# Optimization experiments

Hardware: AMD Instinct MI355X
Metric: run time of the kernel (lower is better)

The kernel has to match this reference:

```python
import jax, jax.numpy as jnp
import numpy as np

NEG = -1e20

def _rope(x):
    # x: (N, L, H, D). Original buffers use inv_freq over D with D/2 entries;
    # sin/cos tiled to full D to broadcast (original code's einsum was under-specified for 4D).
    L, D = x.shape[1], x.shape[3]
    inv_freq = 1.0 / (10000.0 ** (jnp.arange(0, D, 2, dtype=jnp.float32) / D))
    t = jnp.arange(L, dtype=jnp.float32)
    freqs = t[:, None] * inv_freq[None, :]            # (L, D/2)
    sin = jnp.concatenate([jnp.sin(freqs)] * 2, -1)[None, :, None, :]  # (1,L,1,D)
    cos = jnp.concatenate([jnp.cos(freqs)] * 2, -1)[None, :, None, :]
    return x * cos + jnp.flip(x, -1) * sin

def setup_inputs() -> dict:
    key = jax.random.key(0)
    ks = jax.random.split(key, 8)
    N, L, E, H = 2, 1024, 2048, 16
    D = E // H
    s = 0.02
    return {
        "values": jax.random.normal(ks[0], (N, L, E), jnp.float32),
        "keys": jax.random.normal(ks[1], (N, L, E), jnp.float32),
        "queries": jax.random.normal(ks[2], (N, L, E), jnp.float32),
        "mask": jax.random.randint(ks[3], (N, 1, L, L), 0, 2, jnp.int32),
        "Wv": jax.random.normal(ks[4], (D, D), jnp.float32) * s,
        "Wk": jax.random.normal(ks[5], (D, D), jnp.float32) * s,
        "Wq": jax.random.normal(ks[6], (D, D), jnp.float32) * s,
        "Wo": jax.random.normal(ks[7], (E, E), jnp.float32) * s,
        "bo": jnp.zeros((E,), jnp.float32),
    }

def reference(values, keys, queries, mask, Wv, Wk, Wq, Wo, bo):
    N, L, E = queries.shape
    H = 16
    D = E // H
    v = values.reshape(N, L, H, D)
    k = keys.reshape(N, L, H, D)
    q = queries.reshape(N, L, H, D)
    q = _rope(q)
    k = _rope(k)
    # per-head linears (nn.Linear: x @ W.T)
    v = jnp.einsum('nlhd,od->nlho', v, Wv)
    k = jnp.einsum('nlhd,od->nlho', k, Wk)
    q = jnp.einsum('nlhd,od->nlho', q, Wq)
    energy = jnp.einsum('nqhd,nkhd->nhqk', q, k)
    energy = jnp.where(mask == 0, NEG, energy)
    attn = jax.nn.softmax(energy / jnp.sqrt(jnp.float32(E)), axis=3)
    out = jnp.einsum('nhqk,nkhd->nqhd', attn, v).reshape(N, L, E)
    return out @ Wo.T + bo
```

## Files before the change

### kernel.cpp

```cpp
#include <hip/hip_runtime.h>

#define LQ 1024
#define EMB 2048
#define NH 16
#define HD 128
#define RSCALE 0.022097086912079608f

typedef unsigned short u16x8 __attribute__((ext_vector_type(8)));
typedef __bf16 bf16x8 __attribute__((ext_vector_type(8)));
typedef float f32x4 __attribute__((ext_vector_type(4)));
typedef short s16x4 __attribute__((ext_vector_type(4)));

typedef const __attribute__((address_space(1))) unsigned int* gas_t;
typedef __attribute__((address_space(3))) unsigned int* las_t;

__device__ __forceinline__ void glds16(const void* g, void* l){
  __builtin_amdgcn_global_load_lds((gas_t)g, (las_t)l, 16, 0, 0);
}
__device__ __forceinline__ unsigned short f2b(float f){
  unsigned int x = __float_as_uint(f);
  return (unsigned short)((x + 0x7fffu + ((x >> 16) & 1u)) >> 16);
}
__device__ __forceinline__ short f2bs(float f){
  union { __bf16 h; short s; } c; c.h = (__bf16)f; return c.s;
}
__device__ __forceinline__ bf16x8 as_bf(u16x8 u){
  union { u16x8 u; bf16x8 b; } c; c.u = u; return c.b;
}
__device__ __forceinline__ f32x4 mfma16(s16x4 a, s16x4 b, f32x4 c){
  return __builtin_amdgcn_mfma_f32_16x16x16bf16_1k(a, b, c, 0, 0, 0);
}

__global__ __launch_bounds__(256) void k_prep(const float* __restrict__ Wo,
                                              unsigned short* __restrict__ Wob,
                                              const int* __restrict__ M,
                                              unsigned long long* __restrict__ Mb){
  int bx = blockIdx.x, t = threadIdx.x;
  if (bx < 4096) {
    int i = (bx * 256 + t) * 4;
    float4 f = *(const float4*)&Wo[i];
    ushort4 u;
    u.x = f2b(f.x); u.y = f2b(f.y); u.z = f2b(f.z); u.w = f2b(f.w);
    *(ushort4*)&Wob[i] = u;
  } else {
    int w_idx = (bx - 4096) * 4 + (t >> 6);
    int lane = t & 63;
    int n = w_idx >> 14, row = (w_idx >> 4) & 1023, wc = w_idx & 15;
    int v = M[(size_t)n * (LQ * LQ) + (size_t)row * LQ + wc * 64 + lane];
    unsigned long long b = __ballot(v != 0);
    if (lane == 0) Mb[w_idx] = b;
  }
}

__global__ __launch_bounds__(256) void k_proj(
    const float* __restrict__ vals, const float* __restrict__ keys,
    const float* __restrict__ qrys,
    const float* __restrict__ Wv, const float* __restrict__ Wk,
    const float* __restrict__ Wq,
    unsigned short* __restrict__ vp, unsigned short* __restrict__ kp,
    unsigned short* __restrict__ qp)
{
  __shared__ unsigned short Xs[64 * 136];
  __shared__ unsigned short Ws[128 * 136];
  __shared__ float scC[4 * 128], scS[4 * 128];
  int t = threadIdx.x;
  int which = blockIdx.y;
  const float* X; const float* W; unsigned short* OUT; bool rope;
  if (which == 0)      { X = vals; W = Wv; OUT = vp; rope = false; }
  else if (which == 1) { X = keys; W = Wk; OUT = kp; rope = true;  }
  else                 { X = qrys; W = Wq; OUT = qp; rope = true;  }
  float qs = (which == 2) ? RSCALE : 1.0f;
  int m0 = blockIdx.x * 64;

  #pragma unroll
  for (int i = 0; i < 8; ++i) {
    int ci = t + 256 * i;
    int row = ci >> 4, ch = ci & 15;
    float4 a = *(const float4*)&W[row * 128 + ch * 8];
    float4 b = *(const float4*)&W[row * 128 + ch * 8 + 4];
    u16x8 u;
    u[0]=f2b(a.x); u[1]=f2b(a.y); u[2]=f2b(a.z); u[3]=f2b(a.w);
    u[4]=f2b(b.x); u[5]=f2b(b.y); u[6]=f2b(b.z); u[7]=f2b(b.w);
    *(u16x8*)&Ws[row * 136 + ch * 8] = u;
  }
  if (rope) {
    int l0 = (blockIdx.x * 4) & 1023;
    #pragma unroll
    for (int i = 0; i < 2; ++i) {
      int idx = t + 256 * i;
      int li = idx >> 7, d = idx & 127, j = d & 63;
      float inv = 1.0f / powf(10000.0f, (float)(2 * j) * 0.0078125f);
      float ang = (float)(l0 + li) * inv;
      scC[idx] = cosf(ang);
      scS[idx] = sinf(ang);
    }
  }
  __syncthreads();
  #pragma unroll
  for (int i = 0; i < 8; ++i) {
    int fi = t + 256 * i;
    int row = fi >> 5, dq = (fi & 31) * 4;
    int gr = m0 + row;
    float4 x = *(const float4*)&X[(size_t)gr * HD + dq];
    ushort4 u;
    if (rope) {
      int li = row >> 4;
      float4 xm = *(const float4*)&X[(size_t)gr * HD + (124 - dq)];
      float4 c  = *(const float4*)&scC[li * 128 + dq];
      float4 s  = *(const float4*)&scS[li * 128 + dq];
      u.x = f2b(x.x * c.x + xm.w * s.x);
      u.y = f2b(x.y * c.y + xm.z * s.y);
      u.z = f2b(x.z * c.z + xm.y * s.z);
      u.w = f2b(x.w * c.w + xm.x * s.w);
    } else {
      u.x = f2b(x.x); u.y = f2b(x.y); u.z = f2b(x.z); u.w = f2b(x.w);
    }
    *(ushort4*)&Xs[row * 136 + dq] = u;
  }
  __syncthreads();

  int w = t >> 6, lane = t & 63, quad = lane >> 4, n16 = lane & 15;
  f32x4 of[4][2];
  #pragma unroll
  for (int a = 0; a < 4; ++a)
    { of[a][0] = (f32x4){0.f,0.f,0.f,0.f}; of[a][1] = (f32x4){0.f,0.f,0.f,0.f}; }

  #pragma unroll
  for (int kd = 0; kd < 4; ++kd) {
    bf16x8 bfr[2];
    #pragma unroll
    for (int b2 = 0; b2 < 2; ++b2)
      bfr[b2] = as_bf(*(const u16x8*)&Ws[(w * 32 + b2 * 16 + n16) * 136 + kd * 32 + quad * 8]);
    #pragma unroll
    for (int a = 0; a < 4; ++a) {
      bf16x8 af = as_bf(*(const u16x8*)&Xs[(a * 16 + n16) * 136 + kd * 32 + quad * 8]);
      of[a][0] = __builtin_amdgcn_mfma_f32_16x16x32_bf16(af, bfr[0], of[a][0], 0, 0, 0);
      of[a][1] = __builtin_amdgcn_mfma_f32_16x16x32_bf16(af, bfr[1], of[a][1], 0, 0, 0);
    }
  }

  #pragma unroll
  for (int a = 0; a < 4; ++a) {
    #pragma unroll
    for (int b2 = 0; b2 < 2; ++b2) {
      #pragma unroll
      for (int r = 0; r < 4; ++r) {
        int m = m0 + a * 16 + quad * 4 + r;
        int n = m >> 14, l = (m >> 4) & 1023, h = m & 15;
        int o = w * 32 + b2 * 16 + n16;
        OUT[(((size_t)(n * NH + h)) * LQ + l) * HD + o] = f2b(of[a][b2][r] * qs);
      }
    }
  }
}

__global__ __launch_bounds__(256) void k_vtrans(const unsigned short* __restrict__ vp,
                                                unsigned short* __restrict__ vtF){
  __shared__ unsigned short Ls[64 * 136];
  int t = threadIdx.x;
  int kt = blockIdx.x;
  int l0 = kt * 64;
  size_t base = (size_t)blockIdx.y * LQ * HD;
  #pragma unroll
  for (int i = 0; i < 4; ++i) {
    int ci = t + 256 * i;
    int row = ci >> 4, ch = ci & 15;
    *(u16x8*)&Ls[row * 136 + ch * 8] =
        *(const u16x8*)&vp[base + (size_t)(l0 + row) * HD + ch * 8];
  }
  __syncthreads();
  #pragma unroll
  for (int i = 0; i < 4; ++i) {
    int m = t + 256 * i;
    int b = m >> 5, w5 = m & 31;
    int c = b >> 3, c2 = b & 7;
    int l1 = 2 * w5;
    int qd = l1 >> 4, nn0 = l1 & 15;
    u16x8 pk;
    #pragma unroll
    for (int j = 0; j < 4; ++j)
      pk[j] = Ls[(c * 16 + qd * 4 + j) * 136 + c2 * 16 + nn0];
    #pragma unroll
    for (int j = 0; j < 4; ++j)
      pk[4 + j] = Ls[(c * 16 + qd * 4 + j) * 136 + c2 * 16 + nn0 + 1];
    *(u16x8*)&vtF[base + (size_t)kt * 8192 + (size_t)m * 8] = pk;
  }
}

__global__ __launch_bounds__(512) void k_attn(
    const unsigned short* __restrict__ qp, const unsigned short* __restrict__ kp,
    const unsigned short* __restrict__ vtF, const unsigned long long* __restrict__ Mb,
    unsigned short* __restrict__ ao)
{
  __shared__ unsigned short KsF[2][8192];
  __shared__ unsigned short VsF[2][8192];
  __shared__ float ls[8][16];
  int t = threadIdx.x, w = t >> 6, lane = t & 63, quad = lane >> 4, n16 = lane & 15;
  int grp = w >> 2, wq = w & 3;
  int lin = blockIdx.y * gridDim.x + blockIdx.x;
  int xcd = lin & 7, j = lin >> 3;
  int bh = xcd + 8 * (j >> 4);
  int q0 = (j & 15) * 64;
  int nIdx = bh >> 4, h = bh & 15;
  size_t base = (size_t)bh * LQ * HD;
  const unsigned short* Q = qp + base;
  const unsigned short* K = kp + base;
  const unsigned short* VF = vtF + base;

  bf16x8 qf[4];
  #pragma unroll
  for (int kd = 0; kd < 4; ++kd)
    qf[kd] = as_bf(*(const u16x8*)&Q[(size_t)(q0 + wq * 16 + n16) * HD + kd * 32 + quad * 8]);

  const unsigned long long* MbRow =
      Mb + ((size_t)nIdx * LQ + q0 + wq * 16 + n16) * 16;

  f32x4 of[8];
  #pragma unroll
  for (int c = 0; c < 8; ++c) of[c] = (f32x4){0.f, 0.f, 0.f, 0.f};
  float lp = 0.f;

  for (int p = 0; p < 8; ++p) {
    int k0 = p * 128;
    __syncthreads();
    #pragma unroll
    for (int jj = 0; jj < 2; ++jj) {
      int kt = 2 * p + jj;
      #pragma unroll
      for (int i = 0; i < 2; ++i) {
        int D = t + 512 * i;
        int nn = D & 15, qq = (D >> 4) & 3, cc = (D >> 6) & 3, kd = D >> 8;
        glds16(&K[(size_t)(k0 + jj * 64 + cc * 16 + nn) * HD + (kd * 4 + qq) * 8],
               &KsF[jj][(size_t)D * 8]);
        glds16(&VF[(size_t)kt * 8192 + (size_t)D * 8],
               &VsF[jj][(size_t)D * 8]);
      }
    }
    unsigned long long mq = MbRow[2 * p + grp];
    __syncthreads();

    unsigned long long msh = mq >> (quad * 4);

    f32x4 sf[4];
    #pragma unroll
    for (int c = 0; c < 4; ++c) sf[c] = (f32x4){0.f, 0.f, 0.f, 0.f};
    __builtin_amdgcn_s_setprio(1);
    #pragma unroll
    for (int kd = 0; kd < 4; ++kd) {
      #pragma unroll
      for (int c = 0; c < 4; ++c) {
        bf16x8 kv = as_bf(*(const u16x8*)&KsF[grp][((kd * 4 + c) * 64 + lane) * 8]);
        sf[c] = __builtin_amdgcn_mfma_f32_16x16x32_bf16(kv, qf[kd], sf[c], 0, 0, 0);
      }
    }
    __builtin_amdgcn_s_setprio(0);
    #pragma unroll
    for (int c = 0; c < 4; ++c) {
      s16x4 pa;
      #pragma unroll
      for (int r = 0; r < 4; ++r) {
        int bit = (int)((msh >> (c * 16 + r)) & 1ull);
        float p = bit ? __expf(sf[c][r]) : 0.f;
        lp += p;
        pa[r] = f2bs(p);
      }
      __builtin_amdgcn_s_setprio(1);
      #pragma unroll
      for (int c2 = 0; c2 < 8; ++c2) {
        s16x4 vv = *(const s16x4*)&VsF[grp][((c * 8 + c2) * 64 + lane) * 4];
        of[c2] = mfma16(pa, vv, of[c2]);
      }
      __builtin_amdgcn_s_setprio(0);
    }
  }

  __syncthreads();
  {
    float s = lp;
    s += __shfl_xor(s, 16);
    s += __shfl_xor(s, 32);
    ls[w][n16] = s;
  }
  float* OF = (float*)&KsF[0][0];
  if (grp == 1) {
    #pragma unroll
    for (int c2 = 0; c2 < 8; ++c2) {
      #pragma unroll
      for (int r = 0; r < 4; ++r) {
        OF[(wq * 16 + quad * 4 + r) * 128 + c2 * 16 + n16] = of[c2][r];
      }
    }
  }
  __syncthreads();
  if (grp == 0) {
    float linv[4];
    #pragma unroll
    for (int r = 0; r < 4; ++r)
      linv[r] = 1.0f / fmaxf(ls[wq][quad * 4 + r] + ls[wq + 4][quad * 4 + r], 1e-30f);
    #pragma unroll
    for (int c2 = 0; c2 < 8; ++c2) {
      #pragma unroll
      for (int r = 0; r < 4; ++r) {
        float v = of[c2][r] + OF[(wq * 16 + quad * 4 + r) * 128 + c2 * 16 + n16];
        ao[((size_t)(nIdx * LQ + q0 + wq * 16 + quad * 4 + r)) * EMB + h * HD + c2 * 16 + n16] =
            f2b(v * linv[r]);
      }
    }
  }
}

__global__ __launch_bounds__(256) void k_outproj(
    const unsigned short* __restrict__ ao, const unsigned short* __restrict__ Wob,
    const float* __restrict__ bo, float* __restrict__ out)
{
  __shared__ unsigned short As[2][128 * 64];
  __shared__ unsigned short Bs[2][64 * 64];
  int t = threadIdx.x;
  int w = t >> 6, lane = t & 63, quad = lane >> 4, n16 = lane & 15;
  int wm = w >> 1, wo = w & 1;
  int m0 = blockIdx.x * 128, o0 = blockIdx.y * 64;
  int ub = (t & 192);

  f32x4 of[4][2];
  #pragma unroll
  for (int a = 0; a < 4; ++a)
    { of[a][0] = (f32x4){0.f,0.f,0.f,0.f}; of[a][1] = (f32x4){0.f,0.f,0.f,0.f}; }

  #pragma unroll
  for (int i = 0; i < 4; ++i) {
    int ci = t + 256 * i;
    int row = ci >> 3, ch = (ci & 7) ^ (row & 7);
    glds16(&ao[(size_t)(m0 + row) * EMB + ch * 8], &As[0][(ub + 256 * i) * 8]);
  }
  #pragma unroll
  for (int i = 0; i < 2; ++i) {
    int ci = t + 256 * i;
    int row = ci >> 3, ch = (ci & 7) ^ (row & 7);
    glds16(&Wob[(size_t)(o0 + row) * EMB + ch * 8], &Bs[0][(ub + 256 * i) * 8]);
  }

  for (int kt = 0; kt < 32; ++kt) {
    int cur = kt & 1;
    __syncthreads();
    if (kt < 31) {
      int k1 = (kt + 1) * 64;
      #pragma unroll
      for (int i = 0; i < 4; ++i) {
        int ci = t + 256 * i;
        int row = ci >> 3, ch = (ci & 7) ^ (row & 7);
        glds16(&ao[(size_t)(m0 + row) * EMB + k1 + ch * 8], &As[1 - cur][(ub + 256 * i) * 8]);
      }
      #pragma unroll
      for (int i = 0; i < 2; ++i) {
        int ci = t + 256 * i;
        int row = ci >> 3, ch = (ci & 7) ^ (row & 7);
        glds16(&Wob[(size_t)(o0 + row) * EMB + k1 + ch * 8], &Bs[1 - cur][(ub + 256 * i) * 8]);
      }
    }
    #pragma unroll
    for (int kd = 0; kd < 2; ++kd) {
      int slot0 = (kd * 4 + quad);
      bf16x8 af[4], bf[2];
      #pragma unroll
      for (int a = 0; a < 4; ++a)
        af[a] = as_bf(*(const u16x8*)&As[cur][(wm * 64 + a * 16 + n16) * 64 + (slot0 ^ (n16 & 7)) * 8]);
      #pragma unroll
      for (int b = 0; b < 2; ++b)
        bf[b] = as_bf(*(const u16x8*)&Bs[cur][(wo * 32 + b * 16 + n16) * 64 + (slot0 ^ (n16 & 7)) * 8]);
      #pragma unroll
      for (int a = 0; a < 4; ++a)
        #pragma unroll
        for (int b = 0; b < 2; ++b)
          of[a][b] = __builtin_amdgcn_mfma_f32_16x16x32_bf16(af[a], bf[b], of[a][b], 0, 0, 0);
    }
  }

  float bb[2] = { bo[o0 + wo * 32 + n16], bo[o0 + wo * 32 + 16 + n16] };
  #pragma unroll
  for (int a = 0; a < 4; ++a) {
    #pragma unroll
    for (int b = 0; b < 2; ++b) {
      #pragma unroll
      for (int r = 0; r < 4; ++r) {
        out[(size_t)(m0 + wm * 64 + a * 16 + quad * 4 + r) * EMB
            + o0 + wo * 32 + b * 16 + n16] = of[a][b][r] + bb[b];
      }
    }
  }
}

extern "C" void kernel_launch(void* const* d_in, const int* in_sizes, int n_in,
                              void* d_out, int out_size, void* d_ws, size_t ws_size,
                              hipStream_t stream) {
  (void)in_sizes; (void)n_in; (void)out_size; (void)ws_size;
  const float* vals = (const float*)d_in[0];
  const float* keys = (const float*)d_in[1];
  const float* qrys = (const float*)d_in[2];
  const int*   mask = (const int*)d_in[3];
  const float* Wv   = (const float*)d_in[4];
  const float* Wk   = (const float*)d_in[5];
  const float* Wq   = (const float*)d_in[6];
  const float* Wo   = (const float*)d_in[7];
  const float* bo   = (const float*)d_in[8];
  float* out = (float*)d_out;

  unsigned short* U  = (unsigned short*)d_ws;
  unsigned short* qp = U;
  unsigned short* kp = U + 4194304;
  unsigned short* vp = U + 8388608;
  unsigned short* vtF= U + 12582912;
  unsigned short* ao = U + 16777216;
  unsigned short* Wob= U + 20971520;
  unsigned long long* Mb = (unsigned long long*)(U + 25165824);

  k_prep    <<<dim3(12288),  dim3(256), 0, stream>>>(Wo, Wob, mask, Mb);
  k_proj    <<<dim3(512, 3), dim3(256), 0, stream>>>(vals, keys, qrys, Wv, Wk, Wq,
                                                     vp, kp, qp);
  k_vtrans  <<<dim3(16, 32), dim3(256), 0, stream>>>(vp, vtF);
  k_attn    <<<dim3(16, 32), dim3(512), 0, stream>>>(qp, kp, vtF, Mb, ao);
  k_outproj <<<dim3(16, 32), dim3(256), 0, stream>>>(ao, Wob, bo, out);
}
```

Baseline: 206.2 us.

## Fuse prep and V-transpose into projection kernel, writing V in MFMA layout

Removes the separate prep and V-transpose kernels. The Wo bf16 conversion and mask bit-packing now run as an extra grid slice of the projection kernel. The V projection writes its result straight into the fragment-ordered vtF layout, which drops the intermediate vp buffer and its read-back. This saves two launches and a round trip of V through global memory. In exchange the V-row gather becomes strided, and the prep slice does more serial work per block.

```diff
diff --git a/kernel.cpp b/kernel.cpp
--- a/kernel.cpp
+++ b/kernel.cpp
@@ -31,46 +31,49 @@
   return __builtin_amdgcn_mfma_f32_16x16x16bf16_1k(a, b, c, 0, 0, 0);
 }
 
-__global__ __launch_bounds__(256) void k_prep(const float* __restrict__ Wo,
-                                              unsigned short* __restrict__ Wob,
-                                              const int* __restrict__ M,
-                                              unsigned long long* __restrict__ Mb){
-  int bx = blockIdx.x, t = threadIdx.x;
-  if (bx < 4096) {
-    int i = (bx * 256 + t) * 4;
-    float4 f = *(const float4*)&Wo[i];
-    ushort4 u;
-    u.x = f2b(f.x); u.y = f2b(f.y); u.z = f2b(f.z); u.w = f2b(f.w);
-    *(ushort4*)&Wob[i] = u;
-  } else {
-    int w_idx = (bx - 4096) * 4 + (t >> 6);
-    int lane = t & 63;
-    int n = w_idx >> 14, row = (w_idx >> 4) & 1023, wc = w_idx & 15;
-    int v = M[(size_t)n * (LQ * LQ) + (size_t)row * LQ + wc * 64 + lane];
-    unsigned long long b = __ballot(v != 0);
-    if (lane == 0) Mb[w_idx] = b;
-  }
-}
-
 __global__ __launch_bounds__(256) void k_proj(
     const float* __restrict__ vals, const float* __restrict__ keys,
     const float* __restrict__ qrys,
     const float* __restrict__ Wv, const float* __restrict__ Wk,
     const float* __restrict__ Wq,
-    unsigned short* __restrict__ vp, unsigned short* __restrict__ kp,
-    unsigned short* __restrict__ qp)
+    const float* __restrict__ Wo, const int* __restrict__ M,
+    unsigned short* __restrict__ kp, unsigned short* __restrict__ qp,
+    unsigned short* __restrict__ vtF, unsigned short* __restrict__ Wob,
+    unsigned long long* __restrict__ Mb)
 {
   __shared__ unsigned short Xs[64 * 136];
   __shared__ unsigned short Ws[128 * 136];
   __shared__ float scC[4 * 128], scS[4 * 128];
   int t = threadIdx.x;
   int which = blockIdx.y;
-  const float* X; const float* W; unsigned short* OUT; bool rope;
-  if (which == 0)      { X = vals; W = Wv; OUT = vp; rope = false; }
-  else if (which == 1) { X = keys; W = Wk; OUT = kp; rope = true;  }
-  else                 { X = qrys; W = Wq; OUT = qp; rope = true;  }
+
+  if (which == 3) {
+    int bx = blockIdx.x;
+    #pragma unroll
+    for (int k = 0; k < 8; ++k) {
+      int i = (bx * 2048 + k * 256 + t) * 4;
+      float4 f = *(const float4*)&Wo[i];
+      ushort4 u;
+      u.x = f2b(f.x); u.y = f2b(f.y); u.z = f2b(f.z); u.w = f2b(f.w);
+      *(ushort4*)&Wob[i] = u;
+    }
+    int w = t >> 6, lane = t & 63;
+    #pragma unroll
+    for (int i = 0; i < 16; ++i) {
+      int w_idx = bx * 64 + w * 16 + i;
+      int n = w_idx >> 14, row = (w_idx >> 4) & 1023, wc = w_idx & 15;
+      int v = M[(size_t)n * (LQ * LQ) + (size_t)row * LQ + wc * 64 + lane];
+      unsigned long long b = __ballot(v != 0);
+      if (lane == 0) Mb[w_idx] = b;
+    }
+    return;
+  }
+
+  const float* X; const float* W; bool rope;
+  if (which == 0)      { X = vals; W = Wv; rope = false; }
+  else if (which == 1) { X = keys; W = Wk; rope = true;  }
+  else                 { X = qrys; W = Wq; rope = true;  }
   float qs = (which == 2) ? RSCALE : 1.0f;
-  int m0 = blockIdx.x * 64;
 
   #pragma unroll
   for (int i = 0; i < 8; ++i) {
@@ -96,26 +99,38 @@
     }
   }
   __syncthreads();
-  #pragma unroll
-  for (int i = 0; i < 8; ++i) {
-    int fi = t + 256 * i;
-    int row = fi >> 5, dq = (fi & 31) * 4;
-    int gr = m0 + row;
-    float4 x = *(const float4*)&X[(size_t)gr * HD + dq];
-    ushort4 u;
-    if (rope) {
+  if (which == 0) {
+    int bh = blockIdx.x >> 4, kt = blockIdx.x & 15;
+    int n = bh >> 4, h = bh & 15;
+    #pragma unroll
+    for (int i = 0; i < 8; ++i) {
+      int fi = t + 256 * i;
+      int row = fi >> 5, dq = (fi & 31) * 4;
+      size_t gr = (size_t)n * 16384 + (size_t)(kt * 64 + row) * 16 + h;
+      float4 x = *(const float4*)&X[gr * HD + dq];
+      ushort4 u;
+      u.x = f2b(x.x); u.y = f2b(x.y); u.z = f2b(x.z); u.w = f2b(x.w);
+      *(ushort4*)&Xs[row * 136 + dq] = u;
+    }
+  } else {
+    int m0 = blockIdx.x * 64;
+    #pragma unroll
+    for (int i = 0; i < 8; ++i) {
+      int fi = t + 256 * i;
+      int row = fi >> 5, dq = (fi & 31) * 4;
+      int gr = m0 + row;
+      float4 x = *(const float4*)&X[(size_t)gr * HD + dq];
       int li = row >> 4;
       float4 xm = *(const float4*)&X[(size_t)gr * HD + (124 - dq)];
       float4 c  = *(const float4*)&scC[li * 128 + dq];
       float4 s  = *(const float4*)&scS[li * 128 + dq];
+      ushort4 u;
       u.x = f2b(x.x * c.x + xm.w * s.x);
       u.y = f2b(x.y * c.y + xm.z * s.y);
       u.z = f2b(x.z * c.z + xm.y * s.z);
       u.w = f2b(x.w * c.w + xm.x * s.w);
-    } else {
-      u.x = f2b(x.x); u.y = f2b(x.y); u.z = f2b(x.z); u.w = f2b(x.w);
-    }
-    *(ushort4*)&Xs[row * 136 + dq] = u;
+      *(ushort4*)&Xs[row * 136 + dq] = u;
+    }
   }
   __syncthreads();
 
@@ -139,51 +154,38 @@
     }
   }
 
-  #pragma unroll
-  for (int a = 0; a < 4; ++a) {
-    #pragma unroll
-    for (int b2 = 0; b2 < 2; ++b2) {
-      #pragma unroll
-      for (int r = 0; r < 4; ++r) {
-        int m = m0 + a * 16 + quad * 4 + r;
-        int n = m >> 14, l = (m >> 4) & 1023, h = m & 15;
-        int o = w * 32 + b2 * 16 + n16;
-        OUT[(((size_t)(n * NH + h)) * LQ + l) * HD + o] = f2b(of[a][b2][r] * qs);
-      }
-    }
-  }
-}
-
-__global__ __launch_bounds__(256) void k_vtrans(const unsigned short* __restrict__ vp,
-                                                unsigned short* __restrict__ vtF){
-  __shared__ unsigned short Ls[64 * 136];
-  int t = threadIdx.x;
-  int kt = blockIdx.x;
-  int l0 = kt * 64;
-  size_t base = (size_t)blockIdx.y * LQ * HD;
-  #pragma unroll
-  for (int i = 0; i < 4; ++i) {
-    int ci = t + 256 * i;
-    int row = ci >> 4, ch = ci & 15;
-    *(u16x8*)&Ls[row * 136 + ch * 8] =
-        *(const u16x8*)&vp[base + (size_t)(l0 + row) * HD + ch * 8];
-  }
-  __syncthreads();
-  #pragma unroll
-  for (int i = 0; i < 4; ++i) {
-    int m = t + 256 * i;
-    int b = m >> 5, w5 = m & 31;
-    int c = b >> 3, c2 = b & 7;
-    int l1 = 2 * w5;
-    int qd = l1 >> 4, nn0 = l1 & 15;
-    u16x8 pk;
-    #pragma unroll
-    for (int j = 0; j < 4; ++j)
-      pk[j] = Ls[(c * 16 + qd * 4 + j) * 136 + c2 * 16 + nn0];
-    #pragma unroll
-    for (int j = 0; j < 4; ++j)
-      pk[4 + j] = Ls[(c * 16 + qd * 4 + j) * 136 + c2 * 16 + nn0 + 1];
-    *(u16x8*)&vtF[base + (size_t)kt * 8192 + (size_t)m * 8] = pk;
+  if (which == 0) {
+    int bh = blockIdx.x >> 4, kt = blockIdx.x & 15;
+    size_t vbase = (size_t)bh * (LQ * HD) + (size_t)kt * 8192;
+    #pragma unroll
+    for (int a = 0; a < 4; ++a) {
+      #pragma unroll
+      for (int b2 = 0; b2 < 2; ++b2) {
+        ushort4 u;
+        #pragma unroll
+        for (int r = 0; r < 4; ++r) u = (r==0)?(ushort4){f2b(of[a][b2][0]),0,0,0}:u;
+        u.x = f2b(of[a][b2][0]); u.y = f2b(of[a][b2][1]);
+        u.z = f2b(of[a][b2][2]); u.w = f2b(of[a][b2][3]);
+        *(ushort4*)&vtF[vbase + (size_t)((a * 8 + (w * 2 + b2)) * 256
+                                         + (quad * 16 + n16) * 4)] = u;
+      }
+    }
+  } else {
+    unsigned short* OUT = (which == 1) ? kp : qp;
+    int m0 = blockIdx.x * 64;
+    #pragma unroll
+    for (int a = 0; a < 4; ++a) {
+      #pragma unroll
+      for (int b2 = 0; b2 < 2; ++b2) {
+        #pragma unroll
+        for (int r = 0; r < 4; ++r) {
+          int m = m0 + a * 16 + quad * 4 + r;
+          int n = m >> 14, l = (m >> 4) & 1023, h = m & 15;
+          int o = w * 32 + b2 * 16 + n16;
+          OUT[(((size_t)(n * NH + h)) * LQ + l) * HD + o] = f2b(of[a][b2][r] * qs);
+        }
+      }
+    }
   }
 }
 
@@ -407,16 +409,13 @@
   unsigned short* U  = (unsigned short*)d_ws;
   unsigned short* qp = U;
   unsigned short* kp = U + 4194304;
-  unsigned short* vp = U + 8388608;
   unsigned short* vtF= U + 12582912;
   unsigned short* ao = U + 16777216;
   unsigned short* Wob= U + 20971520;
   unsigned long long* Mb = (unsigned long long*)(U + 25165824);
 
-  k_prep    <<<dim3(12288),  dim3(256), 0, stream>>>(Wo, Wob, mask, Mb);
-  k_proj    <<<dim3(512, 3), dim3(256), 0, stream>>>(vals, keys, qrys, Wv, Wk, Wq,
-                                                     vp, kp, qp);
-  k_vtrans  <<<dim3(16, 32), dim3(256), 0, stream>>>(vp, vtF);
+  k_proj    <<<dim3(512, 4), dim3(256), 0, stream>>>(vals, keys, qrys, Wv, Wk, Wq,
+                                                     Wo, mask, kp, qp, vtF, Wob, Mb);
   k_attn    <<<dim3(16, 32), dim3(512), 0, stream>>>(qp, kp, vtF, Mb, ao);
   k_outproj <<<dim3(16, 32), dim3(256), 0, stream>>>(ao, Wob, bo, out);
 }
```

Result: faster. 196.7 us (-4.6%).
